# Kernel optimization log

Hardware: AMD Instinct MI355X
Metric: run time of the kernel (lower is better)

## Reference

```python
import jax, jax.numpy as jnp
import numpy as np

B, NPG, EPG = 512, 256, 4096   # graphs, nodes/graph, edges/graph
N, E = B * NPG, B * EPG
F_IN, H, T = 128, 64, 18
K = 16
D_LAT = 4 * H + 1  # 257


def _p(key, shape, scale=0.05):
    return jax.random.normal(key, shape, dtype=jnp.float32) * scale


def setup_inputs() -> dict:
    key = jax.random.key(0)
    ks = jax.random.split(key, 32)
    x = jax.random.normal(ks[0], (N, F_IN), dtype=jnp.float32)
    off = jnp.repeat(jnp.arange(B, dtype=jnp.int32) * NPG, EPG)
    src = jax.random.randint(ks[1], (E,), 0, NPG, dtype=jnp.int32) + off
    dst = jax.random.randint(ks[2], (E,), 0, NPG, dtype=jnp.int32) + off
    edge_index = jnp.stack([src, dst])
    batch = jnp.repeat(jnp.arange(B, dtype=jnp.int32), NPG)
    inp = {"x": x, "edge_index": edge_index, "batch": batch, "num_graphs": B}
    dims = [F_IN, H, H, H, H]
    outs = [H, H, H, H, 1]
    for i in range(5):
        inp[f"w{i}"] = _p(ks[3 + i], (outs[i], dims[i]))
        inp[f"b{i}"] = jnp.zeros((outs[i],), jnp.float32)
    inp["conv1_w"] = _p(ks[10], (16, 1, D_LAT))
    inp["conv1_b"] = jnp.zeros((16,), jnp.float32)
    inp["conv2_w"] = _p(ks[11], (32, 16, 5))
    inp["conv2_b"] = jnp.zeros((32,), jnp.float32)
    inp["d1_w"] = _p(ks[12], (32, 128))
    inp["d1_b"] = jnp.zeros((32,), jnp.float32)
    inp["d2_w"] = _p(ks[13], (T, 32))
    inp["d2_b"] = jnp.zeros((T,), jnp.float32)
    return inp


def _dgcnn_forward(x, edge_index, batch, num_graphs,
                   ws, bs, conv1_w, conv1_b, conv2_w, conv2_b,
                   d1_w, d1_b, d2_w, d2_b):
    n_nodes = x.shape[0]
    loops = jnp.arange(n_nodes, dtype=edge_index.dtype)
    src = jnp.concatenate([edge_index[0], loops])
    dst = jnp.concatenate([edge_index[1], loops])
    # degree of src indices (with self-loops), norm = 1/deg gathered at dst
    deg = jax.ops.segment_sum(jnp.ones_like(src, x.dtype), src, num_segments=n_nodes)
    inv_deg_dst = (1.0 / deg)[dst]  # deg >= 1 thanks to self-loops

    hidden = []
    h = x
    for w, b in zip(ws, bs):
        h = h @ w.T + b                       # linear transform [N, out]
        msg = h[src] * inv_deg_dst[:, None]    # gather + degree norm [E+N, out]
        h = jax.ops.segment_sum(msg, dst, num_segments=n_nodes)
        h = jnp.tanh(h)
        hidden.append(h)
    feat = jnp.concatenate(hidden, axis=1)     # [N, 257]

    # global_sort_pool: per-graph descending sort on last channel, take top-k
    npg = n_nodes // num_graphs
    xr = feat.reshape(num_graphs, npg, D_LAT)
    order = jnp.argsort(-xr[:, :, -1], axis=1)[:, :K]         # [B, K]
    topk = jnp.take_along_axis(xr, order[:, :, None], axis=1)  # [B, K, 257]

    # conv1d(1->16, kernel=stride=257) over flattened [B, K*257] == per-slot matmul
    c1 = jnp.einsum('bld,od->bol', topk, conv1_w[:, 0, :]) + conv1_b[None, :, None]
    c1 = jax.nn.relu(c1)                                       # [B, 16, 16]
    p1 = c1.reshape(num_graphs, 16, K // 2, 2).max(axis=-1)    # maxpool1d(2,2) -> [B,16,8]
    c2 = jax.lax.conv_general_dilated(p1, conv2_w, (1,), 'VALID',
                                      dimension_numbers=('NCH', 'OIH', 'NCH'))
    c2 = jax.nn.relu(c2 + conv2_b[None, :, None])              # [B, 32, 4]
    flat = c2.reshape(num_graphs, -1)                          # [B, 128]
    last = jax.nn.relu(flat @ d1_w.T + d1_b)                   # [B, 32]
    out = last @ d2_w.T + d2_b                                 # [B, T] (dropout: eval mode)
    return jax.nn.log_softmax(out, axis=1), out, last


def reference(x, edge_index, batch, num_graphs,
              w0, b0, w1, b1, w2, b2, w3, b3, w4, b4,
              conv1_w, conv1_b, conv2_w, conv2_b,
              d1_w, d1_b, d2_w, d2_b):
    ws = [w0, w1, w2, w3, w4]
    bs = [b0, b1, b2, b3, b4]
    return _dgcnn_forward(x, edge_index, batch, num_graphs, ws, bs,
                          conv1_w, conv1_b, conv2_w, conv2_b,
                          d1_w, d1_b, d2_w, d2_b)
```

## Files before the change

### kernel.cpp

```cpp
#include <hip/hip_runtime.h>
#include <math.h>

#define NPG  256
#define EPG  4096
#define NG   512
#define FIN  128
#define HD   64
#define TOUT 18
#define KTOP 16
#define STB  260
#define STA  68
#define SRCL_CAP (EPG + 3*NPG)
#define E_TOT (NG*EPG)

__launch_bounds__(1024)
__global__ void dgcnn_fused(
    const float* __restrict__ x,
    const int*   __restrict__ ei,
    const float* __restrict__ w0, const float* __restrict__ b0,
    const float* __restrict__ w1, const float* __restrict__ b1,
    const float* __restrict__ w2, const float* __restrict__ b2,
    const float* __restrict__ w3, const float* __restrict__ b3,
    const float* __restrict__ w4, const float* __restrict__ b4,
    const float* __restrict__ c1w, const float* __restrict__ c1b,
    const float* __restrict__ c2w, const float* __restrict__ c2b,
    const float* __restrict__ d1w, const float* __restrict__ d1b,
    const float* __restrict__ d2w, const float* __restrict__ d2b,
    float* __restrict__ out)
{
    __shared__ float s_hB[HD*STB];
    __shared__ float s_hl[NPG*STA];
    __shared__ unsigned char s_srcl[SRCL_CAP] __attribute__((aligned(4)));
    __shared__ int   s_off[NPG+1];
    __shared__ int   s_cnt[NPG];
    __shared__ int   s_outd[NPG];
    __shared__ int   s_cur[NPG];
    __shared__ float s_invdeg[NPG];
    __shared__ float s_lin5[NPG];
    __shared__ float s_h5[NPG];
    __shared__ int   s_sel[KTOP];
    __shared__ float s_head[592];

    const int g = blockIdx.x;
    const int t = threadIdx.x;
    const int lane = t & 63;
    const int wid  = t >> 6;
    const int l4 = lane * 4;
    const int gbase = g * NPG;
    const int* __restrict__ srcg = ei + (size_t)g * EPG;
    const int* __restrict__ dstg = ei + (size_t)E_TOT + (size_t)g * EPG;

    if (t < NPG) { s_cnt[t] = 0; s_outd[t] = 0; }
    __syncthreads();
    for (int e = t; e < EPG; e += 1024) {
        int s = srcg[e] - gbase, d = dstg[e] - gbase;
        atomicAdd(&s_outd[s], 1);
        atomicAdd(&s_cnt[d], 1);
    }
    __syncthreads();
    if (t < NPG) s_invdeg[t] = 1.0f / (float)(s_outd[t] + 1);
    if (wid == 0) {
        int c0 = s_cnt[l4], c1 = s_cnt[l4+1], c2 = s_cnt[l4+2], c3 = s_cnt[l4+3];
        int p0 = (c0+3)&~3, p1 = (c1+3)&~3, p2 = (c2+3)&~3, p3 = (c3+3)&~3;
        int tot = p0+p1+p2+p3;
        int run = tot;
        #pragma unroll
        for (int o = 1; o < 64; o <<= 1) {
            int v = __shfl_up(run, o);
            if (lane >= o) run += v;
        }
        int base = run - tot;
        s_off[l4]   = base;
        s_off[l4+1] = base + p0;
        s_off[l4+2] = base + p0 + p1;
        s_off[l4+3] = base + p0 + p1 + p2;
        if (lane == 63) s_off[NPG] = run;
    }
    __syncthreads();
    if (t < NPG) s_cur[t] = s_off[t];
    __syncthreads();
    for (int e = t; e < EPG; e += 1024) {
        int s = srcg[e] - gbase, d = dstg[e] - gbase;
        int pos = atomicAdd(&s_cur[d], 1);
        s_srcl[pos] = (unsigned char)s;
    }
    __syncthreads();
    if (t < NPG) {
        int pe = s_off[t+1];
        for (int p = s_cur[t]; p < pe; p++) s_srcl[p] = (unsigned char)t;
    }
    __syncthreads();

    float projacc[4][4];
    #pragma unroll
    for (int i = 0; i < 4; i++)
        #pragma unroll
        for (int j = 0; j < 4; j++) projacc[i][j] = 0.f;

    auto aggregate = [&]() {
        const int js = lane >> 4;
        const int q4 = (lane & 15) * 4;
        for (int job = wid; job < 64; job += 16) {
            int d   = job*4 + js;
            int off = s_off[d], pe = s_off[d+1];
            int npad = (pe - off) - s_cnt[d];
            float4 a = *(const float4*)&s_hl[d*STA + (q4 ^ (((d>>2)&7)<<2))];
            float cf = (float)(1 - npad);
            a.x *= cf; a.y *= cf; a.z *= cf; a.w *= cf;
            for (int e = off; e < pe; e += 4) {
                unsigned int sq = *(const unsigned int*)&s_srcl[e];
                #pragma unroll
                for (int m = 0; m < 4; m++) {
                    int src = (sq >> (8*m)) & 255;
                    float4 hv = *(const float4*)&s_hl[src*STA + (q4 ^ (((src>>2)&7)<<2))];
                    a.x += hv.x; a.y += hv.y; a.z += hv.z; a.w += hv.w;
                }
            }
            float id = s_invdeg[d];
            s_hB[(q4+0)*STB + d] = tanhf(a.x * id);
            s_hB[(q4+1)*STB + d] = tanhf(a.y * id);
            s_hB[(q4+2)*STB + d] = tanhf(a.z * id);
            s_hB[(q4+3)*STB + d] = tanhf(a.w * id);
        }
    };

    auto matmul64 = [&](const float* __restrict__ w, const float* __restrict__ b) {
        const int c0 = __builtin_amdgcn_readfirstlane(wid * 4);
        const float* wp = w + c0 * HD;
        float acc[4][4];
        #pragma unroll
        for (int i = 0; i < 4; i++)
            #pragma unroll
            for (int j = 0; j < 4; j++) acc[i][j] = 0.f;
        #pragma unroll 8
        for (int k = 0; k < HD; k++) {
            float4 xv = *(const float4*)&s_hB[k*STB + l4];
            float wv0 = wp[k], wv1 = wp[HD+k], wv2 = wp[2*HD+k], wv3 = wp[3*HD+k];
            float xa[4] = {xv.x, xv.y, xv.z, xv.w};
            #pragma unroll
            for (int i = 0; i < 4; i++) {
                acc[i][0] += xa[i]*wv0; acc[i][1] += xa[i]*wv1;
                acc[i][2] += xa[i]*wv2; acc[i][3] += xa[i]*wv3;
            }
        }
        float4 bb = *(const float4*)&b[c0];
        float ba[4] = {bb.x, bb.y, bb.z, bb.w};
        int colb = (wid*4) ^ ((lane & 7) << 2);
        #pragma unroll
        for (int i = 0; i < 4; i++) {
            float4 v;
            v.x = acc[i][0]+ba[0]; v.y = acc[i][1]+ba[1];
            v.z = acc[i][2]+ba[2]; v.w = acc[i][3]+ba[3];
            *(float4*)&s_hl[(l4+i)*STA + colb] = v;
        }
    };

    auto projpass = [&](int Loff) {
        const int o0 = __builtin_amdgcn_readfirstlane(wid * 4);
        const float* p = c1w + o0*257 + Loff;
        #pragma unroll 8
        for (int k = 0; k < HD; k++) {
            float4 xv = *(const float4*)&s_hB[k*STB + l4];
            float p0 = p[k], p1 = p[257+k], p2 = p[514+k], p3 = p[771+k];
            float xa[4] = {xv.x, xv.y, xv.z, xv.w};
            #pragma unroll
            for (int i = 0; i < 4; i++) {
                projacc[i][0] += xa[i]*p0; projacc[i][1] += xa[i]*p1;
                projacc[i][2] += xa[i]*p2; projacc[i][3] += xa[i]*p3;
            }
        }
    };

    {
        const int c0 = __builtin_amdgcn_readfirstlane(wid * 4);
        float acc[4][4];
        #pragma unroll
        for (int i = 0; i < 4; i++)
            #pragma unroll
            for (int j = 0; j < 4; j++) acc[i][j] = 0.f;
        for (int c2 = 0; c2 < 2; c2++) {
            {
                int kk = (t & 15) * 4, nb = t >> 4;
                #pragma unroll
                for (int r = 0; r < 4; r++) {
                    int nn = nb + r*64;
                    float4 v = *(const float4*)&x[(size_t)(gbase+nn)*FIN + c2*64 + kk];
                    s_hB[(kk+0)*STB + nn] = v.x;
                    s_hB[(kk+1)*STB + nn] = v.y;
                    s_hB[(kk+2)*STB + nn] = v.z;
                    s_hB[(kk+3)*STB + nn] = v.w;
                }
            }
            __syncthreads();
            const float* wp = w0 + c0*FIN + c2*64;
            #pragma unroll 8
            for (int k = 0; k < 64; k++) {
                float4 xv = *(const float4*)&s_hB[k*STB + l4];
                float wv0 = wp[k], wv1 = wp[FIN+k], wv2 = wp[2*FIN+k], wv3 = wp[3*FIN+k];
                float xa[4] = {xv.x, xv.y, xv.z, xv.w};
                #pragma unroll
                for (int i = 0; i < 4; i++) {
                    acc[i][0] += xa[i]*wv0; acc[i][1] += xa[i]*wv1;
                    acc[i][2] += xa[i]*wv2; acc[i][3] += xa[i]*wv3;
                }
            }
            __syncthreads();
        }
        float4 bb = *(const float4*)&b0[c0];
        float ba[4] = {bb.x, bb.y, bb.z, bb.w};
        int colb = (wid*4) ^ ((lane & 7) << 2);
        #pragma unroll
        for (int i = 0; i < 4; i++) {
            float4 v;
            v.x = acc[i][0]+ba[0]; v.y = acc[i][1]+ba[1];
            v.z = acc[i][2]+ba[2]; v.w = acc[i][3]+ba[3];
            *(float4*)&s_hl[(l4+i)*STA + colb] = v;
        }
    }
    __syncthreads();
    aggregate();
    __syncthreads();

    if (wid < 4) projpass(0);
    matmul64(w1, b1);
    __syncthreads();
    aggregate();
    __syncthreads();

    if (wid < 4) projpass(64);
    matmul64(w2, b2);
    __syncthreads();
    aggregate();
    __syncthreads();

    if (wid < 4) projpass(128);
    matmul64(w3, b3);
    __syncthreads();
    aggregate();
    __syncthreads();

    if (wid < 4) {
        projpass(192);
    } else if (wid < 8) {
        int n = t - 256;
        float a = b4[0];
        #pragma unroll 8
        for (int k = 0; k < HD; k++) a += s_hB[k*STB + n] * w4[k];
        s_lin5[n] = a;
    }
    __syncthreads();
    if (t < NPG) {
        int d = t;
        int off = s_off[d], pe = s_off[d+1];
        int npad = (pe - off) - s_cnt[d];
        float a = (float)(1 - npad) * s_lin5[d];
        for (int e = off; e < pe; e += 4) {
            unsigned int sq = *(const unsigned int*)&s_srcl[e];
            a += s_lin5[sq & 255] + s_lin5[(sq>>8)&255]
               + s_lin5[(sq>>16)&255] + s_lin5[(sq>>24)&255];
        }
        s_h5[d] = tanhf(a * s_invdeg[d]);
    }
    __syncthreads();
    if (wid < 4) {
        const int o0 = __builtin_amdgcn_readfirstlane(wid * 4);
        float cw0 = c1w[(o0+0)*257 + 256];
        float cw1 = c1w[(o0+1)*257 + 256];
        float cw2 = c1w[(o0+2)*257 + 256];
        float cw3 = c1w[(o0+3)*257 + 256];
        #pragma unroll
        for (int i = 0; i < 4; i++) {
            float hv = s_h5[l4+i];
            float4 v;
            v.x = projacc[i][0] + hv*cw0;
            v.y = projacc[i][1] + hv*cw1;
            v.z = projacc[i][2] + hv*cw2;
            v.w = projacc[i][3] + hv*cw3;
            *(float4*)&s_hl[(l4+i)*16 + wid*4] = v;
        }
    }
    if (wid == 0) {
        float v[4]; int idx[4];
        #pragma unroll
        for (int j = 0; j < 4; j++) { idx[j] = l4+j; v[j] = s_h5[l4+j]; }
        for (int r = 0; r < KTOP; r++) {
            float bv = v[0]; int bi = idx[0];
            #pragma unroll
            for (int j = 1; j < 4; j++)
                if (v[j] > bv || (v[j] == bv && idx[j] < bi)) { bv = v[j]; bi = idx[j]; }
            #pragma unroll
            for (int o = 32; o > 0; o >>= 1) {
                float ov = __shfl_xor(bv, o);
                int   oi = __shfl_xor(bi, o);
                if (ov > bv || (ov == bv && oi < bi)) { bv = ov; bi = oi; }
            }
            if ((bi >> 2) == lane) v[bi & 3] = -1e30f;
            if (lane == 0) s_sel[r] = bi;
        }
    }
    __syncthreads();

    float* s_c1   = s_head;
    float* s_p1   = s_head + 256;
    float* s_flat = s_head + 384;
    float* s_last = s_head + 512;
    float* s_outv = s_head + 544;

    if (t < 256) {
        int sl = t >> 4, o = t & 15;
        float vv = s_hl[s_sel[sl]*16 + o] + c1b[o];
        s_c1[o*16 + sl] = fmaxf(vv, 0.f);
    }
    __syncthreads();
    if (t < 128) {
        int o = t >> 3, j = t & 7;
        s_p1[o*8 + j] = fmaxf(s_c1[o*16 + 2*j], s_c1[o*16 + 2*j + 1]);
    }
    __syncthreads();
    if (t < 128) {
        int oc = t >> 2, tt = t & 3;
        float a = c2b[oc];
        #pragma unroll
        for (int ic = 0; ic < 16; ic++)
            #pragma unroll
            for (int kk = 0; kk < 5; kk++)
                a += s_p1[ic*8 + tt + kk] * c2w[(oc*16 + ic)*5 + kk];
        s_flat[oc*4 + tt] = fmaxf(a, 0.f);
    }
    __syncthreads();
    if (t < 32) {
        float a = d1b[t];
        #pragma unroll 16
        for (int i = 0; i < 128; i++) a += s_flat[i] * d1w[t*128 + i];
        a = fmaxf(a, 0.f);
        s_last[t] = a;
        out[2*NG*TOUT + g*32 + t] = a;
    }
    __syncthreads();
    if (t < TOUT) {
        float a = d2b[t];
        #pragma unroll
        for (int j = 0; j < 32; j++) a += s_last[j] * d2w[t*32 + j];
        s_outv[t] = a;
        out[NG*TOUT + g*TOUT + t] = a;
    }
    __syncthreads();
    if (t < TOUT) {
        float m = s_outv[0];
        for (int i = 1; i < TOUT; i++) m = fmaxf(m, s_outv[i]);
        float sum = 0.f;
        for (int i = 0; i < TOUT; i++) sum += expf(s_outv[i] - m);
        out[g*TOUT + t] = s_outv[t] - m - logf(sum);
    }
}

extern "C" void kernel_launch(void* const* d_in, const int* in_sizes, int n_in,
                              void* d_out, int out_size, void* d_ws, size_t ws_size,
                              hipStream_t stream) {
    (void)in_sizes; (void)n_in; (void)out_size; (void)d_ws; (void)ws_size;
    const float* x   = (const float*)d_in[0];
    const int*   ei  = (const int*)  d_in[1];
    const float* w0  = (const float*)d_in[4];  const float* b0 = (const float*)d_in[5];
    const float* w1  = (const float*)d_in[6];  const float* b1 = (const float*)d_in[7];
    const float* w2  = (const float*)d_in[8];  const float* b2 = (const float*)d_in[9];
    const float* w3  = (const float*)d_in[10]; const float* b3 = (const float*)d_in[11];
    const float* w4  = (const float*)d_in[12]; const float* b4 = (const float*)d_in[13];
    const float* c1w = (const float*)d_in[14]; const float* c1b = (const float*)d_in[15];
    const float* c2w = (const float*)d_in[16]; const float* c2b = (const float*)d_in[17];
    const float* d1w = (const float*)d_in[18]; const float* d1b = (const float*)d_in[19];
    const float* d2w = (const float*)d_in[20]; const float* d2b = (const float*)d_in[21];
    float* out = (float*)d_out;

    dgcnn_fused<<<NG, 1024, 0, stream>>>(x, ei,
        w0, b0, w1, b1, w2, b2, w3, b3, w4, b4,
        c1w, c1b, c2w, c2b, d1w, d1b, d2w, d2b, out);
}
```

Before: 180.5 us.

## Shrink block to 512 threads with row-per-thread matmuls and single LDS buffer

```diff
diff --git a/kernel.cpp b/kernel.cpp
--- a/kernel.cpp
+++ b/kernel.cpp
@@ -8,12 +8,14 @@
 #define HD   64
 #define TOUT 18
 #define KTOP 16
-#define STB  260
-#define STA  68
 #define SRCL_CAP (EPG + 3*NPG)
 #define E_TOT (NG*EPG)
 
-__launch_bounds__(1024)
+__device__ __forceinline__ int hlidx(int n, int c) {
+    return (n << 6) + (c ^ ((n & 7) << 2));
+}
+
+__launch_bounds__(512, 4)
 __global__ void dgcnn_fused(
     const float* __restrict__ x,
     const int*   __restrict__ ei,
@@ -28,31 +30,36 @@
     const float* __restrict__ d2w, const float* __restrict__ d2b,
     float* __restrict__ out)
 {
-    __shared__ float s_hB[HD*STB];
-    __shared__ float s_hl[NPG*STA];
+    __shared__ float s_hl[NPG*64];
     __shared__ unsigned char s_srcl[SRCL_CAP] __attribute__((aligned(4)));
     __shared__ int   s_off[NPG+1];
     __shared__ int   s_cnt[NPG];
-    __shared__ int   s_outd[NPG];
-    __shared__ int   s_cur[NPG];
     __shared__ float s_invdeg[NPG];
     __shared__ float s_lin5[NPG];
     __shared__ float s_h5[NPG];
     __shared__ int   s_sel[KTOP];
     __shared__ float s_head[592];
-
-    const int g = blockIdx.x;
-    const int t = threadIdx.x;
+    int* s_cur  = (int*)s_head;
+    int* s_outd = (int*)(s_head + 256);
+
+    const int g    = blockIdx.x;
+    const int t    = threadIdx.x;
     const int lane = t & 63;
     const int wid  = t >> 6;
-    const int l4 = lane * 4;
+    const int nw   = wid & 3;
+    const int wg   = wid >> 2;
+    const int n    = nw*64 + lane;
+    const int cbase = __builtin_amdgcn_readfirstlane(wg * 32);
+    const int obase = __builtin_amdgcn_readfirstlane(wg * 8);
+    const int js   = lane >> 4;
+    const int q4   = (lane & 15) << 2;
     const int gbase = g * NPG;
     const int* __restrict__ srcg = ei + (size_t)g * EPG;
     const int* __restrict__ dstg = ei + (size_t)E_TOT + (size_t)g * EPG;
 
     if (t < NPG) { s_cnt[t] = 0; s_outd[t] = 0; }
     __syncthreads();
-    for (int e = t; e < EPG; e += 1024) {
+    for (int e = t; e < EPG; e += 512) {
         int s = srcg[e] - gbase, d = dstg[e] - gbase;
         atomicAdd(&s_outd[s], 1);
         atomicAdd(&s_cnt[d], 1);
@@ -60,9 +67,10 @@
     __syncthreads();
     if (t < NPG) s_invdeg[t] = 1.0f / (float)(s_outd[t] + 1);
     if (wid == 0) {
-        int c0 = s_cnt[l4], c1 = s_cnt[l4+1], c2 = s_cnt[l4+2], c3 = s_cnt[l4+3];
-        int p0 = (c0+3)&~3, p1 = (c1+3)&~3, p2 = (c2+3)&~3, p3 = (c3+3)&~3;
-        int tot = p0+p1+p2+p3;
+        int p4 = lane * 4;
+        int c0 = s_cnt[p4], c1 = s_cnt[p4+1], c2 = s_cnt[p4+2], c3 = s_cnt[p4+3];
+        int q0 = (c0+3)&~3, q1 = (c1+3)&~3, q2 = (c2+3)&~3, q3 = (c3+3)&~3;
+        int tot = q0+q1+q2+q3;
         int run = tot;
         #pragma unroll
         for (int o = 1; o < 64; o <<= 1) {
@@ -70,16 +78,16 @@
             if (lane >= o) run += v;
         }
         int base = run - tot;
-        s_off[l4]   = base;
-        s_off[l4+1] = base + p0;
-        s_off[l4+2] = base + p0 + p1;
-        s_off[l4+3] = base + p0 + p1 + p2;
+        s_off[p4]   = base;
+        s_off[p4+1] = base + q0;
+        s_off[p4+2] = base + q0 + q1;
+        s_off[p4+3] = base + q0 + q1 + q2;
         if (lane == 63) s_off[NPG] = run;
     }
     __syncthreads();
     if (t < NPG) s_cur[t] = s_off[t];
     __syncthreads();
-    for (int e = t; e < EPG; e += 1024) {
+    for (int e = t; e < EPG; e += 512) {
         int s = srcg[e] - gbase, d = dstg[e] - gbase;
         int pos = atomicAdd(&s_cur[d], 1);
         s_srcl[pos] = (unsigned char)s;
@@ -91,198 +99,142 @@
     }
     __syncthreads();
 
-    float projacc[4][4];
-    #pragma unroll
-    for (int i = 0; i < 4; i++)
-        #pragma unroll
-        for (int j = 0; j < 4; j++) projacc[i][j] = 0.f;
-
-    auto aggregate = [&]() {
-        const int js = lane >> 4;
-        const int q4 = (lane & 15) * 4;
-        for (int job = wid; job < 64; job += 16) {
-            int d   = job*4 + js;
+    auto runAgg = [&]() {
+        float4 res[8];
+        #pragma unroll
+        for (int r = 0; r < 8; r++) {
+            int d = r*32 + wid*4 + js;
             int off = s_off[d], pe = s_off[d+1];
             int npad = (pe - off) - s_cnt[d];
-            float4 a = *(const float4*)&s_hl[d*STA + (q4 ^ (((d>>2)&7)<<2))];
+            float4 a = *(const float4*)&s_hl[hlidx(d, q4)];
             float cf = (float)(1 - npad);
             a.x *= cf; a.y *= cf; a.z *= cf; a.w *= cf;
             for (int e = off; e < pe; e += 4) {
-                unsigned int sq = *(const unsigned int*)&s_srcl[e];
+                unsigned sq = *(const unsigned*)&s_srcl[e];
                 #pragma unroll
                 for (int m = 0; m < 4; m++) {
                     int src = (sq >> (8*m)) & 255;
-                    float4 hv = *(const float4*)&s_hl[src*STA + (q4 ^ (((src>>2)&7)<<2))];
+                    float4 hv = *(const float4*)&s_hl[hlidx(src, q4)];
                     a.x += hv.x; a.y += hv.y; a.z += hv.z; a.w += hv.w;
                 }
             }
             float id = s_invdeg[d];
-            s_hB[(q4+0)*STB + d] = tanhf(a.x * id);
-            s_hB[(q4+1)*STB + d] = tanhf(a.y * id);
-            s_hB[(q4+2)*STB + d] = tanhf(a.z * id);
-            s_hB[(q4+3)*STB + d] = tanhf(a.w * id);
-        }
+            res[r].x = tanhf(a.x * id); res[r].y = tanhf(a.y * id);
+            res[r].z = tanhf(a.z * id); res[r].w = tanhf(a.w * id);
+        }
+        __syncthreads();
+        #pragma unroll
+        for (int r = 0; r < 8; r++) {
+            int d = r*32 + wid*4 + js;
+            *(float4*)&s_hl[hlidx(d, q4)] = res[r];
+        }
+        __syncthreads();
     };
 
-    auto matmul64 = [&](const float* __restrict__ w, const float* __restrict__ b) {
-        const int c0 = __builtin_amdgcn_readfirstlane(wid * 4);
-        const float* wp = w + c0 * HD;
-        float acc[4][4];
-        #pragma unroll
-        for (int i = 0; i < 4; i++)
-            #pragma unroll
-            for (int j = 0; j < 4; j++) acc[i][j] = 0.f;
-        #pragma unroll 8
-        for (int k = 0; k < HD; k++) {
-            float4 xv = *(const float4*)&s_hB[k*STB + l4];
-            float wv0 = wp[k], wv1 = wp[HD+k], wv2 = wp[2*HD+k], wv3 = wp[3*HD+k];
-            float xa[4] = {xv.x, xv.y, xv.z, xv.w};
-            #pragma unroll
-            for (int i = 0; i < 4; i++) {
-                acc[i][0] += xa[i]*wv0; acc[i][1] += xa[i]*wv1;
-                acc[i][2] += xa[i]*wv2; acc[i][3] += xa[i]*wv3;
-            }
-        }
-        float4 bb = *(const float4*)&b[c0];
-        float ba[4] = {bb.x, bb.y, bb.z, bb.w};
-        int colb = (wid*4) ^ ((lane & 7) << 2);
-        #pragma unroll
-        for (int i = 0; i < 4; i++) {
-            float4 v;
-            v.x = acc[i][0]+ba[0]; v.y = acc[i][1]+ba[1];
-            v.z = acc[i][2]+ba[2]; v.w = acc[i][3]+ba[3];
-            *(float4*)&s_hl[(l4+i)*STA + colb] = v;
-        }
-    };
-
-    auto projpass = [&](int Loff) {
-        const int o0 = __builtin_amdgcn_readfirstlane(wid * 4);
-        const float* p = c1w + o0*257 + Loff;
-        #pragma unroll 8
-        for (int k = 0; k < HD; k++) {
-            float4 xv = *(const float4*)&s_hB[k*STB + l4];
-            float p0 = p[k], p1 = p[257+k], p2 = p[514+k], p3 = p[771+k];
-            float xa[4] = {xv.x, xv.y, xv.z, xv.w};
-            #pragma unroll
-            for (int i = 0; i < 4; i++) {
-                projacc[i][0] += xa[i]*p0; projacc[i][1] += xa[i]*p1;
-                projacc[i][2] += xa[i]*p2; projacc[i][3] += xa[i]*p3;
-            }
-        }
-    };
-
     {
-        const int c0 = __builtin_amdgcn_readfirstlane(wid * 4);
-        float acc[4][4];
-        #pragma unroll
-        for (int i = 0; i < 4; i++)
-            #pragma unroll
-            for (int j = 0; j < 4; j++) acc[i][j] = 0.f;
-        for (int c2 = 0; c2 < 2; c2++) {
-            {
-                int kk = (t & 15) * 4, nb = t >> 4;
-                #pragma unroll
-                for (int r = 0; r < 4; r++) {
-                    int nn = nb + r*64;
-                    float4 v = *(const float4*)&x[(size_t)(gbase+nn)*FIN + c2*64 + kk];
-                    s_hB[(kk+0)*STB + nn] = v.x;
-                    s_hB[(kk+1)*STB + nn] = v.y;
-                    s_hB[(kk+2)*STB + nn] = v.z;
-                    s_hB[(kk+3)*STB + nn] = v.w;
-                }
-            }
-            __syncthreads();
-            const float* wp = w0 + c0*FIN + c2*64;
-            #pragma unroll 8
-            for (int k = 0; k < 64; k++) {
-                float4 xv = *(const float4*)&s_hB[k*STB + l4];
-                float wv0 = wp[k], wv1 = wp[FIN+k], wv2 = wp[2*FIN+k], wv3 = wp[3*FIN+k];
-                float xa[4] = {xv.x, xv.y, xv.z, xv.w};
-                #pragma unroll
-                for (int i = 0; i < 4; i++) {
-                    acc[i][0] += xa[i]*wv0; acc[i][1] += xa[i]*wv1;
-                    acc[i][2] += xa[i]*wv2; acc[i][3] += xa[i]*wv3;
-                }
-            }
-            __syncthreads();
-        }
-        float4 bb = *(const float4*)&b0[c0];
-        float ba[4] = {bb.x, bb.y, bb.z, bb.w};
-        int colb = (wid*4) ^ ((lane & 7) << 2);
-        #pragma unroll
-        for (int i = 0; i < 4; i++) {
-            float4 v;
-            v.x = acc[i][0]+ba[0]; v.y = acc[i][1]+ba[1];
-            v.z = acc[i][2]+ba[2]; v.w = acc[i][3]+ba[3];
-            *(float4*)&s_hl[(l4+i)*STA + colb] = v;
-        }
-    }
-    __syncthreads();
-    aggregate();
-    __syncthreads();
-
-    if (wid < 4) projpass(0);
-    matmul64(w1, b1);
-    __syncthreads();
-    aggregate();
-    __syncthreads();
-
-    if (wid < 4) projpass(64);
-    matmul64(w2, b2);
-    __syncthreads();
-    aggregate();
-    __syncthreads();
-
-    if (wid < 4) projpass(128);
-    matmul64(w3, b3);
-    __syncthreads();
-    aggregate();
-    __syncthreads();
-
-    if (wid < 4) {
-        projpass(192);
-    } else if (wid < 8) {
-        int n = t - 256;
-        float a = b4[0];
-        #pragma unroll 8
-        for (int k = 0; k < HD; k++) a += s_hB[k*STB + n] * w4[k];
-        s_lin5[n] = a;
-    }
-    __syncthreads();
-    if (t < NPG) {
-        int d = t;
-        int off = s_off[d], pe = s_off[d+1];
-        int npad = (pe - off) - s_cnt[d];
-        float a = (float)(1 - npad) * s_lin5[d];
-        for (int e = off; e < pe; e += 4) {
-            unsigned int sq = *(const unsigned int*)&s_srcl[e];
-            a += s_lin5[sq & 255] + s_lin5[(sq>>8)&255]
-               + s_lin5[(sq>>16)&255] + s_lin5[(sq>>24)&255];
-        }
-        s_h5[d] = tanhf(a * s_invdeg[d]);
-    }
-    __syncthreads();
-    if (wid < 4) {
-        const int o0 = __builtin_amdgcn_readfirstlane(wid * 4);
-        float cw0 = c1w[(o0+0)*257 + 256];
-        float cw1 = c1w[(o0+1)*257 + 256];
-        float cw2 = c1w[(o0+2)*257 + 256];
-        float cw3 = c1w[(o0+3)*257 + 256];
-        #pragma unroll
-        for (int i = 0; i < 4; i++) {
-            float hv = s_h5[l4+i];
-            float4 v;
-            v.x = projacc[i][0] + hv*cw0;
-            v.y = projacc[i][1] + hv*cw1;
-            v.z = projacc[i][2] + hv*cw2;
-            v.w = projacc[i][3] + hv*cw3;
-            *(float4*)&s_hl[(l4+i)*16 + wid*4] = v;
-        }
-    }
+        float acc[32];
+        #pragma unroll
+        for (int c = 0; c < 32; c++) acc[c] = b0[cbase + c];
+        const float* xrow = x + (size_t)(gbase + n) * FIN;
+        for (int kq = 0; kq < 32; kq++) {
+            float4 hv = *(const float4*)&xrow[kq*4];
+            #pragma unroll
+            for (int c = 0; c < 32; c++) {
+                float4 wq = *(const float4*)&w0[(cbase+c)*FIN + kq*4];
+                acc[c] += hv.x*wq.x + hv.y*wq.y + hv.z*wq.z + hv.w*wq.w;
+            }
+        }
+        #pragma unroll
+        for (int j = 0; j < 8; j++) {
+            float4 v = {acc[4*j], acc[4*j+1], acc[4*j+2], acc[4*j+3]};
+            *(float4*)&s_hl[hlidx(n, cbase + 4*j)] = v;
+        }
+    }
+    __syncthreads();
+    runAgg();
+
+    float proj[8];
+    #pragma unroll
+    for (int o = 0; o < 8; o++) proj[o] = 0.f;
+
+    #pragma unroll 1
+    for (int L = 1; L <= 3; L++) {
+        const float* w = (L==1) ? w1 : (L==2) ? w2 : w3;
+        const float* b = (L==1) ? b1 : (L==2) ? b2 : b3;
+        const int loff = (L-1)*64;
+        float acc[32];
+        #pragma unroll
+        for (int c = 0; c < 32; c++) acc[c] = b[cbase + c];
+        for (int kq = 0; kq < 16; kq++) {
+            float4 hv = *(const float4*)&s_hl[hlidx(n, kq*4)];
+            #pragma unroll
+            for (int c = 0; c < 32; c++) {
+                float4 wq = *(const float4*)&w[(cbase+c)*HD + kq*4];
+                acc[c] += hv.x*wq.x + hv.y*wq.y + hv.z*wq.z + hv.w*wq.w;
+            }
+            #pragma unroll
+            for (int o = 0; o < 8; o++) {
+                const float* cp = c1w + (obase+o)*257 + loff + kq*4;
+                proj[o] += hv.x*cp[0] + hv.y*cp[1] + hv.z*cp[2] + hv.w*cp[3];
+            }
+        }
+        __syncthreads();
+        #pragma unroll
+        for (int j = 0; j < 8; j++) {
+            float4 v = {acc[4*j], acc[4*j+1], acc[4*j+2], acc[4*j+3]};
+            *(float4*)&s_hl[hlidx(n, cbase + 4*j)] = v;
+        }
+        __syncthreads();
+        runAgg();
+    }
+
+    {
+        float lin5 = b4[0];
+        for (int kq = 0; kq < 16; kq++) {
+            float4 hv = *(const float4*)&s_hl[hlidx(n, kq*4)];
+            if (wg == 0) {
+                lin5 += hv.x*w4[kq*4] + hv.y*w4[kq*4+1]
+                      + hv.z*w4[kq*4+2] + hv.w*w4[kq*4+3];
+            }
+            #pragma unroll
+            for (int o = 0; o < 8; o++) {
+                const float* cp = c1w + (obase+o)*257 + 192 + kq*4;
+                proj[o] += hv.x*cp[0] + hv.y*cp[1] + hv.z*cp[2] + hv.w*cp[3];
+            }
+        }
+        if (wg == 0) s_lin5[n] = lin5;
+        __syncthreads();
+        if (t < NPG) {
+            int d = t;
+            int off = s_off[d], pe = s_off[d+1];
+            int npad = (pe - off) - s_cnt[d];
+            float a = (float)(1 - npad) * s_lin5[d];
+            for (int e = off; e < pe; e += 4) {
+                unsigned sq = *(const unsigned*)&s_srcl[e];
+                a += s_lin5[sq & 255] + s_lin5[(sq>>8)&255]
+                   + s_lin5[(sq>>16)&255] + s_lin5[(sq>>24)&255];
+            }
+            s_h5[d] = tanhf(a * s_invdeg[d]);
+        }
+        __syncthreads();
+        {
+            float h5 = s_h5[n];
+            #pragma unroll
+            for (int o = 0; o < 8; o++) proj[o] += h5 * c1w[(obase+o)*257 + 256];
+        }
+        #pragma unroll
+        for (int j = 0; j < 2; j++) {
+            float4 v = {proj[4*j], proj[4*j+1], proj[4*j+2], proj[4*j+3]};
+            *(float4*)&s_hl[hlidx(n, obase + 4*j)] = v;
+        }
+    }
+    __syncthreads();
+
     if (wid == 0) {
         float v[4]; int idx[4];
-        #pragma unroll
-        for (int j = 0; j < 4; j++) { idx[j] = l4+j; v[j] = s_h5[l4+j]; }
+        int p4 = lane * 4;
+        #pragma unroll
+        for (int j = 0; j < 4; j++) { idx[j] = p4 + j; v[j] = s_h5[p4 + j]; }
         for (int r = 0; r < KTOP; r++) {
             float bv = v[0]; int bi = idx[0];
             #pragma unroll
@@ -308,7 +260,8 @@
 
     if (t < 256) {
         int sl = t >> 4, o = t & 15;
-        float vv = s_hl[s_sel[sl]*16 + o] + c1b[o];
+        int sn = s_sel[sl];
+        float vv = s_hl[hlidx(sn, o)] + c1b[o];
         s_c1[o*16 + sl] = fmaxf(vv, 0.f);
     }
     __syncthreads();
@@ -371,7 +324,7 @@
     const float* d2w = (const float*)d_in[20]; const float* d2b = (const float*)d_in[21];
     float* out = (float*)d_out;
 
-    dgcnn_fused<<<NG, 1024, 0, stream>>>(x, ei,
+    dgcnn_fused<<<NG, 512, 0, stream>>>(x, ei,
         w0, b0, w1, b1, w2, b2, w3, b3, w4, b4,
         c1w, c1b, c2w, c2b, d1w, d1b, d2w, d2b, out);
 }
```

Result: slower. 224.9 us, median of 2 (+24.6%).
